# Kernel tuning notes

Measured on AMD Instinct MI355X. Metric: run time of the kernel, lower is better.

The kernel has to match this reference:

```python
import jax, jax.numpy as jnp
import numpy as np

B, T, N_ITEMS, DIM, L = 512, 50, 10000, 128, 4
H = DIM // 2


def setup_inputs() -> dict:
    key = jax.random.key(0)
    ks = jax.random.split(key, 16)
    emb = jax.random.normal(ks[0], (N_ITEMS + 1, DIM), jnp.float32) * 0.02
    emb = emb.at[0].set(0.0)  # padding_idx=0
    s = 1.0 / np.sqrt(DIM)
    inp = {
        "users": jax.random.randint(ks[1], (B,), 0, B),
        "user_seq": jax.random.randint(ks[2], (B, T), 0, N_ITEMS + 1),
        "pos_items": jax.random.randint(ks[3], (B,), 0, N_ITEMS),
        "neg_items": jax.random.randint(ks[4], (B, 10), 0, N_ITEMS),
        "pos_labels": jnp.ones((B,), jnp.float32),
        "neg_labels": jnp.zeros((B, 10), jnp.float32),
        "base_model_preds": jax.random.normal(ks[5], (B, N_ITEMS), jnp.float32),
        "emb": emb,
        "lstm_wih": jax.random.uniform(ks[6], (4 * DIM, DIM), jnp.float32, -s, s),
        "lstm_whh": jax.random.uniform(ks[7], (4 * DIM, DIM), jnp.float32, -s, s),
        "lstm_bih": jax.random.uniform(ks[8], (4 * DIM,), jnp.float32, -s, s),
        "lstm_bhh": jax.random.uniform(ks[9], (4 * DIM,), jnp.float32, -s, s),
        "wl_W1": jax.random.normal(ks[10], (L, 2 * DIM, H), jnp.float32) * 0.05,
        "wl_b1": jax.random.normal(ks[11], (L, H), jnp.float32) * 0.01,
        "wl_W2": jax.random.normal(ks[12], (L, H), jnp.float32) * 0.05,
        "wl_b2": jax.random.normal(ks[13], (L,), jnp.float32) * 0.01,
        "alphas": jnp.ones((L,), jnp.float32) / L,
    }
    return inp


def _lstm_last(x, wih, whh, bih, bhh):
    # x: [B, T, D]; torch gate order i, f, g, o. Returns last hidden state [B, D].
    Bx, _, D = x.shape
    bias = bih + bhh

    def step(carry, xt):
        h, c = carry
        gates = xt @ wih.T + h @ whh.T + bias  # [B, 4D]
        i, f, g, o = jnp.split(gates, 4, axis=-1)
        c = jax.nn.sigmoid(f) * c + jax.nn.sigmoid(i) * jnp.tanh(g)
        h = jax.nn.sigmoid(o) * jnp.tanh(c)
        return (h, c), None

    init = (jnp.zeros((Bx, D), x.dtype), jnp.zeros((Bx, D), x.dtype))
    (h, _), _ = jax.lax.scan(step, init, x.transpose(1, 0, 2))
    return h


def reference(users, user_seq, pos_items, neg_items, pos_labels, neg_labels,
              base_model_preds, emb, lstm_wih, lstm_whh, lstm_bih, lstm_bhh,
              wl_W1, wl_b1, wl_W2, wl_b2, alphas):
    seq_emb = emb[user_seq]                      # [B, T, D]
    seq_repr = _lstm_last(seq_emb, lstm_wih, lstm_whh, lstm_bih, lstm_bhh)  # [B, D]
    item_emb = emb[jnp.arange(N_ITEMS)]          # [N, D]

    # Weak learners: Linear(2D->H) split algebraically into seq/item matmuls
    # to avoid materializing the [B, N, 2D] broadcast-concat tensor.
    final_scores = jnp.zeros((seq_repr.shape[0], N_ITEMS), seq_repr.dtype)
    for l in range(L):
        sp = seq_repr @ wl_W1[l, :DIM]           # [B, H]
        ip = item_emb @ wl_W1[l, DIM:]           # [N, H]
        hid = jax.nn.relu(sp[:, None, :] + ip[None, :, :] + wl_b1[l])  # [B, N, H]
        scores = hid @ wl_W2[l] + wl_b2[l]       # [B, N]
        final_scores = final_scores + alphas[l] * scores

    pos_scores = jnp.take_along_axis(final_scores, pos_items[:, None], axis=1)  # [B, 1]
    neg_scores = jnp.take_along_axis(final_scores, neg_items, axis=1)           # [B, n_neg]
    loss = jnp.mean(jnp.exp(-(pos_scores - neg_scores)))
    return final_scores, loss
```

## Files before the change

kernel.cpp:

```cpp
#include <hip/hip_runtime.h>
#include <stdint.h>

typedef uint32_t u32;
typedef uint16_t u16;
typedef uint64_t u64;
typedef __attribute__((ext_vector_type(4))) float f32x4;
typedef __attribute__((ext_vector_type(4))) u32 u32x4;
typedef __attribute__((ext_vector_type(8))) short bf16x8;
typedef __attribute__((ext_vector_type(2))) _Float16 f16x2;

#define NI   10000
#define NPAD 10240
#define L2E  1.4426950408889634f

#define DEV static __device__ __forceinline__

DEV float asf(u32 u){ union{u32 i; float f;} v; v.i=u; return v.f; }
DEV u32   asu(float f){ union{u32 i; float f;} v; v.f=f; return v.i; }
DEV float bf2f(u16 u){ return asf(((u32)u)<<16); }
DEV u16   f2bf(float f){ u32 i = asu(f); return (u16)((i + 0x7fffu + ((i>>16)&1u))>>16); }
DEV u16   f2h(float f){ _Float16 h = (_Float16)f; return __builtin_bit_cast(u16, h); }
DEV f32x4 fzero(){ f32x4 z; z[0]=0.f; z[1]=0.f; z[2]=0.f; z[3]=0.f; return z; }

DEV void gl2lds16(const void* g, void* l){
  __builtin_amdgcn_global_load_lds((const __attribute__((address_space(1))) u32*)g,
                                   (__attribute__((address_space(3))) u32*)l, 16, 0, 0);
}

__global__ void k_prep(const int* __restrict__ seq, const float* __restrict__ emb,
                       const float* __restrict__ wih, const float* __restrict__ bih,
                       const float* __restrict__ bhh, const float* __restrict__ W1,
                       const float* __restrict__ b1, const float* __restrict__ W2,
                       const float* __restrict__ alphas,
                       u16* __restrict__ EMB16, u16* __restrict__ Wih16,
                       u16* __restrict__ W1s16, u16* __restrict__ W1i16,
                       float* __restrict__ bias512, float* __restrict__ b1k,
                       u32* __restrict__ w2p)
{
  const int tid = blockIdx.x*blockDim.x + threadIdx.x;
  const int nth = gridDim.x*blockDim.x;
  for (int e = tid; e < 10001*16; e += nth){
    const float* s = emb + (size_t)e*8;
    float4 x0 = *(const float4*)s, x1 = *(const float4*)(s+4);
    bf16x8 o;
    o[0]=(short)f2bf(x0.x); o[1]=(short)f2bf(x0.y); o[2]=(short)f2bf(x0.z); o[3]=(short)f2bf(x0.w);
    o[4]=(short)f2bf(x1.x); o[5]=(short)f2bf(x1.y); o[6]=(short)f2bf(x1.z); o[7]=(short)f2bf(x1.w);
    *(bf16x8*)&EMB16[(size_t)e*8] = o;
  }
  for (int e = tid; e < 512*16; e += nth){
    int col = (e*8)>>7;
    float sc = ((col>>7)==2) ? 2.0f*L2E : L2E;
    const float* s = wih + (size_t)e*8;
    float4 x0 = *(const float4*)s, x1 = *(const float4*)(s+4);
    bf16x8 o;
    o[0]=(short)f2bf(x0.x*sc); o[1]=(short)f2bf(x0.y*sc); o[2]=(short)f2bf(x0.z*sc); o[3]=(short)f2bf(x0.w*sc);
    o[4]=(short)f2bf(x1.x*sc); o[5]=(short)f2bf(x1.y*sc); o[6]=(short)f2bf(x1.z*sc); o[7]=(short)f2bf(x1.w*sc);
    *(bf16x8*)&Wih16[(size_t)e*8] = o;
  }
  for (int e = tid; e < 256*128; e += nth){ int k = e>>7, d = e&127; int l = k>>6, h = k&63;
      W1s16[e] = f2bf(W1[l*16384 + d*64 + h]); }
  for (int e = tid; e < 256*128; e += nth){ int k = e>>7, d = e&127; int l = k>>6, h = k&63;
      W1i16[e] = f2bf(W1[l*16384 + (128+d)*64 + h]); }
  for (int e = tid; e < 512; e += nth){
      float sc = ((e>>7)==2) ? 2.0f*L2E : L2E;
      bias512[e] = (bih[e] + bhh[e])*sc; }
  for (int e = tid; e < 256; e += nth){ int l = e>>6, h = e&63;
      b1k[e] = b1[l*64 + h]; }
  for (int e = tid; e < 128; e += nth){
      int k0 = 2*e, k1 = 2*e+1;
      float w0 = alphas[k0>>6]*W2[(k0>>6)*64 + (k0&63)];
      float w1 = alphas[k1>>6]*W2[(k1>>6)*64 + (k1&63)];
      w2p[e] = (u32)f2h(w0) | ((u32)f2h(w1)<<16); }
}

template<int OUT_MODE, int BIAS_MODE>
DEV void gemm_body(const u16* __restrict__ A, const u16* __restrict__ BT,
                   const float* __restrict__ bias, void* __restrict__ Cout,
                   int Nvalid, int ldc, int bx, int by, char* smem,
                   const int* __restrict__ seq)
{
  u16* sA = (u16*)smem;
  u16* sB = (u16*)(smem + 32768);
  const int tid = threadIdx.x, l = tid&63, w = tid>>6;
  const int c16 = l&15, g4 = l>>4;
  const int m0 = bx*128, n0 = by*64;
  #pragma unroll
  for (int it=0; it<4; ++it){
    int row = it*32 + w*4 + g4;
    int sg  = c16 ^ (row&7);
    if constexpr (OUT_MODE==4){
      int b = (m0&511) + row, t = m0>>9;
      int idx = seq[b*50 + t];
      gl2lds16(A + (size_t)idx*128 + sg*8, (char*)sA + (it*32 + w*4)*256);
    } else {
      gl2lds16(A + (size_t)(m0+row)*128 + sg*8, (char*)sA + (it*32 + w*4)*256);
    }
  }
  #pragma unroll
  for (int it=0; it<2; ++it){
    int row = it*32 + w*4 + g4;
    int srow;
    if constexpr (OUT_MODE==4){
      int base1 = (by>>2)*256 + (by&3)*32;
      srow = base1 + (row&31) + (row>>5)*128;
    } else {
      srow = n0 + row; if (srow >= Nvalid) srow = Nvalid-1;
    }
    int sg  = c16 ^ (row&7);
    gl2lds16(BT + (size_t)srow*128 + sg*8, (char*)sB + (it*32 + w*4)*256);
  }
  __syncthreads();
  f32x4 acc[4];
  #pragma unroll
  for (int ct=0; ct<4; ++ct) acc[ct] = fzero();
  #pragma unroll
  for (int kt=0; kt<4; ++kt){
    bf16x8 a, b[4];
    int arow = w*16 + c16;
    a = *(const bf16x8*)((const char*)sA + arow*256 + (((kt*4+g4) ^ (arow&7))*16));
    #pragma unroll
    for (int ct=0; ct<4; ++ct){
      int brow = (OUT_MODE==4) ? ((ct>>1)*32 + (ct&1)*16 + c16) : (ct*16 + c16);
      b[ct] = *(const bf16x8*)((const char*)sB + brow*256 + (((kt*4+g4) ^ (brow&7))*16));
    }
    #pragma unroll
    for (int ct=0; ct<4; ++ct)
      acc[ct] = __builtin_amdgcn_mfma_f32_16x16x32_bf16(a, b[ct], acc[ct], 0, 0, 0);
  }
  const int rbase = m0 + w*16 + g4*4;
  if constexpr (OUT_MODE==4){
    int t    = rbase >> 9;
    int bloc = rbase & 511;
    int bb   = bloc >> 4;
    int g4l  = (bloc >> 2) & 3;
    int half = by >> 2;
    #pragma unroll
    for (int p=0; p<2; ++p){
      int colA = (by&3)*32 + p*16 + c16 + (by>>2)*256;
      int colB = colA + 128;
      u32 ws[4];
      #pragma unroll
      for (int i=0;i<4;++i){
        float va = acc[p][i], vb = acc[p+2][i];
        if constexpr (BIAS_MODE==1){ va += bias[colA]; vb += bias[colB]; }
        ws[i] = (u32)f2bf(va) | ((u32)f2bf(vb)<<16);
      }
      int tidl = ((by&3)*2 + p)*64 + g4l*16 + c16;
      char* dst = (char*)Cout + ((size_t)((t*32+bb)*1024 + half*512 + tidl))*16;
      *(f32x4*)dst = *(f32x4*)ws;
    }
  } else {
    #pragma unroll
    for (int ct=0; ct<4; ++ct){
      int col = n0 + ct*16 + c16;
      if (col < Nvalid){
        float v[4];
        #pragma unroll
        for (int i=0;i<4;++i){
          v[i] = acc[ct][i];
          if constexpr (BIAS_MODE==1) v[i] += bias[col];
          else if constexpr (BIAS_MODE==2) v[i] += bias[rbase+i];
        }
        if constexpr (OUT_MODE==0){
          float* C = (float*)Cout;
          #pragma unroll
          for (int i=0;i<4;++i) C[(size_t)(rbase+i)*ldc + col] = v[i];
        } else if constexpr (OUT_MODE==1){
          u16* C = (u16*)Cout;
          #pragma unroll
          for (int i=0;i<4;++i) C[(size_t)(rbase+i)*ldc + col] = f2h(v[i]);
        } else {
          u32* C = (u32*)Cout;
          u32 w0 = (u32)f2h(v[0]) | ((u32)f2h(v[1])<<16);
          u32 w1 = (u32)f2h(v[2]) | ((u32)f2h(v[3])<<16);
          int kp0 = rbase>>1;
          C[(size_t)kp0*ldc + col]     = w0;
          C[(size_t)(kp0+1)*ldc + col] = w1;
        }
      }
    }
  }
}

template<int OUT_MODE, int BIAS_MODE>
__global__ __launch_bounds__(512) void k_gemm(const u16* __restrict__ A,
    const u16* __restrict__ BT, const float* __restrict__ bias,
    void* __restrict__ Cout, int Nvalid, int ldc, const int* __restrict__ seq)
{
  __shared__ __align__(16) char smem[49152];
  gemm_body<OUT_MODE,BIAS_MODE>(A, BT, bias, Cout, Nvalid, ldc, blockIdx.x, blockIdx.y, smem, seq);
}

DEV void lstm_body(const float* __restrict__ whh, const u16* __restrict__ XWL,
                   u16* __restrict__ H16, int bb, char* smem)
{
  const int tid = threadIdx.x, l = tid&63, w = tid>>6;
  const int c16 = l&15, g4 = l>>4;
  const int u = w*16 + c16;
  bf16x8 bfr[4][4];
  #pragma unroll
  for (int j=0; j<4; ++j){
    int col = (j*8 + w)*16 + c16;
    float sc = (j==2) ? 2.0f*L2E : L2E;
    const float* src = whh + (size_t)col*128;
    #pragma unroll
    for (int kt=0; kt<4; ++kt){
      int k0 = kt*32 + g4*8;
      float4 x0 = *(const float4*)(src + k0);
      float4 x1 = *(const float4*)(src + k0 + 4);
      bf16x8 f;
      f[0]=(short)f2bf(x0.x*sc); f[1]=(short)f2bf(x0.y*sc); f[2]=(short)f2bf(x0.z*sc); f[3]=(short)f2bf(x0.w*sc);
      f[4]=(short)f2bf(x1.x*sc); f[5]=(short)f2bf(x1.y*sc); f[6]=(short)f2bf(x1.z*sc); f[7]=(short)f2bf(x1.w*sc);
      bfr[kt][j] = f;
    }
  }
  for (int e = tid; e < 4096; e += 512) ((u16*)smem)[e] = 0;
  int hoff[4];
  #pragma unroll
  for (int i=0;i<4;++i){ int s = g4*4 + i;
    hoff[i] = s*256 + (((u>>3) ^ (s&7))*16) + (u&7)*2; }
  const char* gb = (const char*)XWL;
  {
    size_t base = (size_t)bb*1024;
    gl2lds16(gb + (base + tid)*16,        smem + 8192 + w*1024);
    gl2lds16(gb + (base + 512 + tid)*16,  smem + 8192 + 8192 + w*1024);
  }
  float cst[4] = {0.f,0.f,0.f,0.f};
  float hreg[4] = {0.f,0.f,0.f,0.f};
  __syncthreads();
  #pragma unroll 2
  for (int t=0; t<50; ++t){
    const int cur = t&1;
    char* AhC = smem + cur*4096;
    char* AhN = smem + (cur^1)*4096;
    char* XsC = smem + 8192 + cur*16384;
    char* XsN = smem + 8192 + (cur^1)*16384;
    if (t < 49){
      size_t base = (size_t)((t+1)*32+bb)*1024;
      gl2lds16(gb + (base + tid)*16,       XsN + w*1024);
      gl2lds16(gb + (base + 512 + tid)*16, XsN + 8192 + w*1024);
    }
    bf16x8 xv0 = *(const bf16x8*)(XsC + tid*16);
    bf16x8 xv1 = *(const bf16x8*)(XsC + 8192 + tid*16);
    const u32* W0 = (const u32*)&xv0;
    const u32* W1 = (const u32*)&xv1;
    f32x4 acc[4];
    #pragma unroll
    for (int i=0;i<4;++i){
      acc[0][i] = asf(W0[i]<<16);
      acc[1][i] = asf(W0[i]&0xffff0000u);
      acc[2][i] = asf(W1[i]<<16);
      acc[3][i] = asf(W1[i]&0xffff0000u);
    }
    #pragma unroll
    for (int kt=0; kt<4; ++kt){
      bf16x8 a = *(const bf16x8*)(AhC + c16*256 + (((kt*4+g4) ^ (c16&7))*16));
      #pragma unroll
      for (int j=0; j<4; ++j)
        acc[j] = __builtin_amdgcn_mfma_f32_16x16x32_bf16(a, bfr[kt][j], acc[j], 0, 0, 0);
    }
    #pragma unroll
    for (int i=0;i<4;++i){
      float yi = acc[0][i], yf = acc[1][i], yg = acc[2][i], yo = acc[3][i];
      yg = fminf(fmaxf(yg, -40.f), 40.f);
      float Ei = __builtin_amdgcn_exp2f(-yi);
      float Ef = __builtin_amdgcn_exp2f(-yf);
      float G  = __builtin_amdgcn_exp2f(yg);
      float Eo = __builtin_amdgcn_exp2f(-yo);
      float ai = 1.f+Ei, af = 1.f+Ef, gp = G+1.f, gm = G-1.f;
      float num = fmaf(af, gm, cst[i]*ai*gp);
      float den = af*ai*gp;
      float cn  = num * __builtin_amdgcn_rcpf(den);
      cst[i] = cn;
      float yc = fminf(fmaxf(cn*(2.0f*L2E), -40.f), 40.f);
      float C2 = __builtin_amdgcn_exp2f(yc);
      float h  = (C2-1.f) * __builtin_amdgcn_rcpf((1.f+Eo)*(C2+1.f));
      hreg[i] = h;
      *(u16*)(AhN + hoff[i]) = f2bf(h);
    }
    __syncthreads();
  }
  #pragma unroll
  for (int i=0;i<4;++i)
    H16[(size_t)(bb*16 + g4*4 + i)*128 + u] = f2bf(hreg[i]);
}

__global__ __launch_bounds__(512) void k_lstm_ipf(const float* __restrict__ whh,
    const u16* __restrict__ XWL, u16* __restrict__ H16,
    const u16* __restrict__ W1i16, const u16* __restrict__ EMB16,
    const float* __restrict__ b1k, u32* __restrict__ IPF)
{
  __shared__ __align__(16) char smem[49152];
  if (blockIdx.x < 32){
    lstm_body(whh, XWL, H16, blockIdx.x, smem);
  } else {
    int g = blockIdx.x - 32;
    gemm_body<2,2>(W1i16, EMB16, b1k, IPF, NI, NPAD, g&1, g>>1, smem, nullptr);
  }
}

__global__ __launch_bounds__(512) void k_post(const u16* __restrict__ H16,
    const u16* __restrict__ W1s16, u16* __restrict__ SPH)
{
  __shared__ __align__(16) char smem[49152];
  gemm_body<1,0>(H16, W1s16, nullptr, SPH, 256, 256, blockIdx.x&3, blockIdx.x>>2, smem, nullptr);
}

DEV float fdot2(u32 ab, u32 w, float acc){
  asm("v_dot2_f32_f16 %0, %1, %2, %0" : "+v"(acc) : "v"(ab), "s"(w));
  return acc;
}
DEV u32 pkmax0(u32 t){
  u32 r; asm("v_pk_max_f16 %0, %1, 0" : "=v"(r) : "v"(t)); return r;
}

__global__ __launch_bounds__(256) void k_score(const u32* __restrict__ SPH,
    const u32* __restrict__ IPF, const u32* __restrict__ w2p,
    const float* __restrict__ alphas, const float* __restrict__ b2,
    float* __restrict__ out)
{
  __shared__ __align__(16) u32 sp_lds[16*128];
  const int tid = threadIdx.x;
  const int n  = blockIdx.x*256 + tid;
  const int b0 = blockIdx.y*16;
  {
    const u32* src = SPH + (size_t)b0*128 + tid*8;
    *(u32x4*)&sp_lds[tid*8]   = *(const u32x4*)src;
    *(u32x4*)&sp_lds[tid*8+4] = *(const u32x4*)(src+4);
  }
  float cb2 = 0.f;
  #pragma unroll
  for (int ll=0;ll<4;++ll) cb2 += alphas[ll]*b2[ll];
  __syncthreads();
  float acc[16];
  #pragma unroll
  for (int i=0;i<16;++i) acc[i] = cb2;
  #pragma unroll 1
  for (int c=0;c<4;++c){
    u32 iw[32];
    #pragma unroll
    for (int v=0; v<32; ++v) iw[v] = IPF[(size_t)(c*32+v)*NPAD + n];
    const u32* wp = w2p + c*32;
    #pragma unroll
    for (int i=0;i<16;++i){
      float a = acc[i];
      #pragma unroll
      for (int vq=0; vq<8; ++vq){
        u32x4 sp4 = *(const u32x4*)&sp_lds[i*128 + c*32 + vq*4];
        #pragma unroll
        for (int q=0;q<4;++q){
          f16x2 t = __builtin_bit_cast(f16x2, sp4[q]) + __builtin_bit_cast(f16x2, iw[vq*4+q]);
          u32 r = pkmax0(__builtin_bit_cast(u32, t));
          a = fdot2(r, wp[vq*4+q], a);
        }
      }
      acc[i] = a;
    }
  }
  if (n < NI){
    #pragma unroll
    for (int i=0;i<16;++i) out[(size_t)(b0+i)*NI + n] = acc[i];
  }
}

__global__ void k_loss(const float* __restrict__ scores, const int* __restrict__ pos,
                       const int* __restrict__ neg, float* __restrict__ outloss)
{
  __shared__ float red[256];
  int tid = threadIdx.x;
  float s = 0.f;
  for (int e = tid; e < 5120; e += 256){
    int b = e/10, j = e - b*10;
    float ps = scores[(size_t)b*NI + pos[b]];
    float ns = scores[(size_t)b*NI + neg[b*10 + j]];
    s += __expf(ns - ps);
  }
  red[tid] = s; __syncthreads();
  for (int st=128; st>0; st>>=1){ if (tid<st) red[tid]+=red[tid+st]; __syncthreads(); }
  if (tid==0) outloss[0] = red[0] * (1.0f/5120.0f);
}

extern "C" void kernel_launch(void* const* d_in, const int* in_sizes, int n_in,
                              void* d_out, int out_size, void* d_ws, size_t ws_size,
                              hipStream_t stream)
{
  const int*   seq    = (const int*)d_in[1];
  const int*   pos    = (const int*)d_in[2];
  const int*   neg    = (const int*)d_in[3];
  const float* emb    = (const float*)d_in[7];
  const float* wih    = (const float*)d_in[8];
  const float* whh    = (const float*)d_in[9];
  const float* bih    = (const float*)d_in[10];
  const float* bhh    = (const float*)d_in[11];
  const float* W1     = (const float*)d_in[12];
  const float* b1     = (const float*)d_in[13];
  const float* W2     = (const float*)d_in[14];
  const float* b2     = (const float*)d_in[15];
  const float* alphas = (const float*)d_in[16];
  float* out = (float*)d_out;
  (void)in_sizes; (void)n_in; (void)out_size; (void)ws_size;

  char* p = (char*)d_ws;
  size_t off = 0;
  auto alloc = [&](size_t bytes)->char*{ char* r = p + off;
      off = (off + bytes + 255) & ~(size_t)255; return r; };
  u16*  EMB16   = (u16*)  alloc((size_t)10001*128*2);
  u16*  Wih16   = (u16*)  alloc((size_t)512*128*2);
  u16*  W1s16   = (u16*)  alloc((size_t)256*128*2);
  u16*  W1i16   = (u16*)  alloc((size_t)256*128*2);
  float* bias512= (float*)alloc(512*4);
  float* b1k    = (float*)alloc(256*4);
  u32*  w2p     = (u32*)  alloc(128*4);
  u16*  XWL     = (u16*)  alloc((size_t)25600*512*2);
  u16*  H16     = (u16*)  alloc((size_t)512*128*2);
  u16*  SPH     = (u16*)  alloc((size_t)512*256*2);
  u32*  IPF     = (u32*)  alloc((size_t)128*NPAD*4);

  k_prep<<<512,256,0,stream>>>(seq, emb, wih, bih, bhh, W1, b1, W2, alphas,
                               EMB16, Wih16, W1s16, W1i16, bias512, b1k, w2p);
  k_gemm<4,1><<<dim3(200,8),512,0,stream>>>(EMB16, Wih16, bias512, XWL, 512, 512, seq);
  k_lstm_ipf<<<32 + 314,512,0,stream>>>(whh, XWL, H16, W1i16, EMB16, b1k, IPF);
  k_post<<<16,512,0,stream>>>(H16, W1s16, SPH);
  k_score<<<dim3(40,32),256,0,stream>>>((const u32*)SPH, IPF, w2p, alphas, b2, out);
  k_loss<<<1,256,0,stream>>>(out, pos, neg, out + (size_t)512*NI);
}
```

Baseline: 164.7 us.

## Triple-buffer LSTM input prefetch with two-step lookahead and explicit waitcnt barriers

The LSTM recurrence now keeps three LDS buffers for the precomputed input projections and prefetches two timesteps ahead. __syncthreads is replaced by explicit lgkmcnt and vmcnt waits plus s_barrier, so the loop only waits on the older prefetch and global loads stay in flight across steps. Shared memory grows from 48 KB to 56 KB, which can lower occupancy for the co-scheduled GEMM blocks in the same kernel. k_score also gets a launch-bounds occupancy hint.

```diff
diff --git a/kernel.cpp b/kernel.cpp
--- a/kernel.cpp
+++ b/kernel.cpp
@@ -220,26 +220,32 @@
   for (int i=0;i<4;++i){ int s = g4*4 + i;
     hoff[i] = s*256 + (((u>>3) ^ (s&7))*16) + (u&7)*2; }
   const char* gb = (const char*)XWL;
-  {
-    size_t base = (size_t)bb*1024;
-    gl2lds16(gb + (base + tid)*16,        smem + 8192 + w*1024);
-    gl2lds16(gb + (base + 512 + tid)*16,  smem + 8192 + 8192 + w*1024);
+  #pragma unroll
+  for (int tt=0; tt<2; ++tt){
+    size_t base = (size_t)(tt*32+bb)*1024;
+    gl2lds16(gb + (base + tid)*16,       smem + 8192 + tt*16384 + w*1024);
+    gl2lds16(gb + (base + 512 + tid)*16, smem + 8192 + tt*16384 + 8192 + w*1024);
   }
   float cst[4] = {0.f,0.f,0.f,0.f};
   float hreg[4] = {0.f,0.f,0.f,0.f};
-  __syncthreads();
-  #pragma unroll 2
+  asm volatile("s_waitcnt lgkmcnt(0)" ::: "memory");
+  asm volatile("s_waitcnt vmcnt(2)" ::: "memory");
+  __builtin_amdgcn_s_barrier();
+  __builtin_amdgcn_sched_barrier(0);
+  int cur = 0;
+  #pragma unroll 1
   for (int t=0; t<50; ++t){
-    const int cur = t&1;
-    char* AhC = smem + cur*4096;
-    char* AhN = smem + (cur^1)*4096;
+    char* AhC = smem + (t&1)*4096;
+    char* AhN = smem + ((t&1)^1)*4096;
     char* XsC = smem + 8192 + cur*16384;
-    char* XsN = smem + 8192 + (cur^1)*16384;
-    if (t < 49){
-      size_t base = (size_t)((t+1)*32+bb)*1024;
-      gl2lds16(gb + (base + tid)*16,       XsN + w*1024);
-      gl2lds16(gb + (base + 512 + tid)*16, XsN + 8192 + w*1024);
-    }
+    if (t < 48){
+      int nxt2 = (cur+2 >= 3) ? cur-1 : cur+2;
+      char* XsP = smem + 8192 + nxt2*16384;
+      size_t base = (size_t)((t+2)*32+bb)*1024;
+      gl2lds16(gb + (base + tid)*16,       XsP + w*1024);
+      gl2lds16(gb + (base + 512 + tid)*16, XsP + 8192 + w*1024);
+    }
+    __builtin_amdgcn_sched_barrier(0);
     bf16x8 xv0 = *(const bf16x8*)(XsC + tid*16);
     bf16x8 xv1 = *(const bf16x8*)(XsC + 8192 + tid*16);
     const u32* W0 = (const u32*)&xv0;
@@ -278,7 +284,12 @@
       hreg[i] = h;
       *(u16*)(AhN + hoff[i]) = f2bf(h);
     }
-    __syncthreads();
+    asm volatile("s_waitcnt lgkmcnt(0)" ::: "memory");
+    if (t < 48) asm volatile("s_waitcnt vmcnt(2)" ::: "memory");
+    else        asm volatile("s_waitcnt vmcnt(0)" ::: "memory");
+    __builtin_amdgcn_s_barrier();
+    __builtin_amdgcn_sched_barrier(0);
+    cur = (cur+1 == 3) ? 0 : cur+1;
   }
   #pragma unroll
   for (int i=0;i<4;++i)
@@ -290,7 +301,7 @@
     const u16* __restrict__ W1i16, const u16* __restrict__ EMB16,
     const float* __restrict__ b1k, u32* __restrict__ IPF)
 {
-  __shared__ __align__(16) char smem[49152];
+  __shared__ __align__(16) char smem[57344];
   if (blockIdx.x < 32){
     lstm_body(whh, XWL, H16, blockIdx.x, smem);
   } else {
@@ -314,7 +325,7 @@
   u32 r; asm("v_pk_max_f16 %0, %1, 0" : "=v"(r) : "v"(t)); return r;
 }
 
-__global__ __launch_bounds__(256) void k_score(const u32* __restrict__ SPH,
+__global__ __launch_bounds__(256, 4) void k_score(const u32* __restrict__ SPH,
     const u32* __restrict__ IPF, const u32* __restrict__ w2p,
     const float* __restrict__ alphas, const float* __restrict__ b2,
     float* __restrict__ out)
```

Result: slower. 169.8 us (+3.1%).
